# Kernel optimization log

Measured on AMD Instinct MI355X. Metric: run time of the kernel, lower is better.

Reference implementation:

```python
import jax, jax.numpy as jnp
import numpy as np

B_, L_, D_MODEL = 2, 4096, 1024
D_STATE, D_CONV, D_INNER = 64, 4, 2048
EPS = 1.1920929e-07  # torch.finfo(float32).eps, nn.RMSNorm default


def setup_inputs() -> dict:
    key = jax.random.key(0)
    ks = jax.random.split(key, 8)
    s = 0.02
    x = jax.random.normal(ks[0], (B_, L_, D_MODEL), jnp.float32)
    W_in = jax.random.normal(ks[1], (D_MODEL, 2 * D_INNER), jnp.float32) * s
    conv_w = jax.random.normal(ks[2], (D_INNER, 1, D_CONV), jnp.float32) * s  # depthwise (O,I/g,K)
    conv_b = jnp.zeros((D_INNER,), jnp.float32)
    W_x = jax.random.normal(ks[3], (D_INNER, 2 * D_STATE + D_INNER), jnp.float32) * s
    W_dt = jax.random.normal(ks[4], (D_INNER, D_INNER), jnp.float32) * s
    b_dt = jnp.zeros((D_INNER,), jnp.float32)
    A_log = jnp.log(jnp.tile(jnp.arange(1, D_STATE + 1, dtype=jnp.float32)[None, :], (D_INNER, 1)))
    D_param = jnp.ones((D_INNER,), jnp.float32)
    W_out = jax.random.normal(ks[5], (D_INNER, D_MODEL), jnp.float32) * s
    norm_w = jnp.ones((D_INNER,), jnp.float32)
    return dict(x=x, W_in=W_in, conv_w=conv_w, conv_b=conv_b, W_x=W_x, W_dt=W_dt,
                b_dt=b_dt, A_log=A_log, D_param=D_param, W_out=W_out, norm_w=norm_w)


def selective_scan(x_conv, dt, A, B_ssm, C_ssm, D_param):
    # x_conv,dt: (B,L,d_inner); A:(d_inner,d_state); B_ssm,C_ssm:(B,L,d_state)
    dt = jax.nn.softplus(dt)

    def step(h, inp):
        dt_t, B_t, C_t, x_t = inp  # (B,di),(B,ds),(B,ds),(B,di)
        dA = jnp.exp(dt_t[:, :, None] * A[None, :, :])           # (B,di,ds)
        h = dA * h + (dt_t * x_t)[:, :, None] * B_t[:, None, :]  # (B,di,ds)
        y = jnp.einsum('bds,bs->bd', h, C_t)                     # (B,di)
        return h, y

    h0 = jnp.zeros((x_conv.shape[0], A.shape[0], A.shape[1]), x_conv.dtype)
    xs = (jnp.moveaxis(dt, 1, 0), jnp.moveaxis(B_ssm, 1, 0),
          jnp.moveaxis(C_ssm, 1, 0), jnp.moveaxis(x_conv, 1, 0))
    _, ys = jax.lax.scan(step, h0, xs)
    y = jnp.moveaxis(ys, 0, 1)  # (B,L,d_inner)
    return y + x_conv * D_param[None, None, :]


def reference(x, W_in, conv_w, conv_b, W_x, W_dt, b_dt, A_log, D_param, W_out, norm_w):
    xz = x @ W_in                                    # (B,L,2*d_inner)
    x_ssm, z = jnp.split(xz, 2, axis=-1)
    # causal depthwise conv1d: left-pad d_conv-1 == torch pad-both-then-slice[:L]
    xc = jnp.swapaxes(x_ssm, 1, 2)                   # (B,d_inner,L)
    xc = jax.lax.conv_general_dilated(
        xc, conv_w, window_strides=(1,), padding=[(D_CONV - 1, 0)],
        dimension_numbers=('NCH', 'OIH', 'NCH'), feature_group_count=D_INNER)
    xc = xc + conv_b[None, :, None]
    xc = jax.nn.silu(jnp.swapaxes(xc, 1, 2))         # (B,L,d_inner)
    dbc = xc @ W_x                                   # (B,L,2*d_state+d_inner)
    B_ssm = dbc[..., :D_STATE]
    C_ssm = dbc[..., D_STATE:2 * D_STATE]
    dt = dbc[..., 2 * D_STATE:] @ W_dt + b_dt
    A = -jnp.exp(A_log)
    y = selective_scan(xc, dt, A, B_ssm, C_ssm, D_param)
    # RMSNorm then gate
    y = y * jax.lax.rsqrt(jnp.mean(y * y, axis=-1, keepdims=True) + EPS) * norm_w
    y = y * jax.nn.silu(z)
    return y @ W_out
```

## Files before the change

kernel.cpp:

```cpp
#include <hip/hip_runtime.h>
#include <hip/hip_bf16.h>

#define L_SEQ   4096
#define DMODEL  1024
#define DINNER  2048
#define DSTATE  64
#define NB      2
#define DPB     128
#define DBCS    2304
#define NROWS   (NB * L_SEQ)

typedef unsigned short u16;
typedef __attribute__((ext_vector_type(8))) short bf16x8;
typedef __attribute__((ext_vector_type(4))) float f32x4;
typedef __attribute__((ext_vector_type(2))) float f32x2;

__device__ __forceinline__ float silu_f(float x)  { return x / (1.f + __expf(-x)); }
__device__ __forceinline__ float softplus_f(float x) {
    return x > 15.f ? x : __logf(1.f + __expf(x));
}
__device__ __forceinline__ float bf2f(u16 u) { return __uint_as_float(((unsigned)u) << 16); }
__device__ __forceinline__ u16 f2bf(float f) {
    __hip_bfloat16 h = __float2bfloat16(f);
    return *reinterpret_cast<u16*>(&h);
}
__device__ __forceinline__ unsigned pack2(float a, float b) {
    return (unsigned)f2bf(a) | ((unsigned)f2bf(b) << 16);
}

__global__ __launch_bounds__(256) void f32_to_bf16_kernel(
    const float* __restrict__ in, u16* __restrict__ out)
{
    const int i = (blockIdx.x * 256 + threadIdx.x) * 4;
    float4 v = *reinterpret_cast<const float4*>(in + i);
    ushort4 o;
    o.x = f2bf(v.x); o.y = f2bf(v.y); o.z = f2bf(v.z); o.w = f2bf(v.w);
    *reinterpret_cast<ushort4*>(out + i) = o;
}

__global__ __launch_bounds__(256) void transpose_bf16_kernel(
    const float* __restrict__ W, u16* __restrict__ Wt, int K, int N)
{
    __shared__ float t[32][33];
    const int n0 = blockIdx.x * 32, k0 = blockIdx.y * 32;
    const int tx = threadIdx.x & 31, ty = threadIdx.x >> 5;
    #pragma unroll
    for (int i = 0; i < 32; i += 8)
        t[ty + i][tx] = W[(size_t)(k0 + ty + i) * N + n0 + tx];
    __syncthreads();
    #pragma unroll
    for (int i = 0; i < 32; i += 8)
        Wt[(size_t)(n0 + ty + i) * K + k0 + tx] = f2bf(t[tx][ty + i]);
}

__global__ __launch_bounds__(256) void bias_cat_kernel(
    const float* __restrict__ b_dt, float* __restrict__ bias)
{
    const int i = blockIdx.x * 256 + threadIdx.x;
    float v = 0.f;
    if (i >= 128 && i < 128 + DINNER) v = b_dt[i - 128];
    bias[i] = v;
}

template <typename TC>
__global__ __launch_bounds__(256) void mfma_gemm(
    const u16* __restrict__ A, int lda,
    const u16* __restrict__ Bt, int ldb,
    TC* __restrict__ C, int ldc,
    int K, const float* __restrict__ bias)
{
    __shared__ u16 As[128 * 32];
    __shared__ u16 Bs[128 * 32];
    const int tid  = threadIdx.x;
    const int lane = tid & 63;
    const int w    = tid >> 6;
    const int wm   = w >> 1, wn = w & 1;

    const int gx = gridDim.x;
    const int nwg = gx * gridDim.y;
    int wg = blockIdx.y * gx + blockIdx.x;
    if ((nwg & 7) == 0) wg = (wg & 7) * (nwg >> 3) + (wg >> 3);
    const int bm = (wg / gx) * 128, bn = (wg % gx) * 128;

    const int lr = lane & 15, lk = lane >> 4;
    const int srow  = lane >> 2;
    const int scolb = (lane & 3) * 16;
    const size_t ldaB = (size_t)lda * 2, ldbB = (size_t)ldb * 2;

    const char* Ab = (const char*)A + (size_t)bm * ldaB;
    const char* Bb = (const char*)Bt + (size_t)bn * ldbB;
    char* AsB = (char*)As;
    char* BsB = (char*)Bs;

    f32x4 acc[4][4] = {};

    for (int k0 = 0; k0 < K; k0 += 32) {
        const size_t kb = (size_t)k0 * 2;
        #pragma unroll
        for (int i = 0; i < 2; ++i) {
            const int row = i * 64 + w * 16 + srow;
            __builtin_amdgcn_global_load_lds(
                (const __attribute__((address_space(1))) void*)(Ab + (size_t)row * ldaB + kb + scolb),
                (__attribute__((address_space(3))) void*)(AsB + i * 4096 + w * 1024),
                16, 0, 0);
            __builtin_amdgcn_global_load_lds(
                (const __attribute__((address_space(1))) void*)(Bb + (size_t)row * ldbB + kb + scolb),
                (__attribute__((address_space(3))) void*)(BsB + i * 4096 + w * 1024),
                16, 0, 0);
        }
        __syncthreads();
        bf16x8 a[4], b[4];
        #pragma unroll
        for (int mi = 0; mi < 4; ++mi)
            a[mi] = *reinterpret_cast<const bf16x8*>(&As[(wm * 64 + mi * 16 + lr) * 32 + lk * 8]);
        #pragma unroll
        for (int ni = 0; ni < 4; ++ni)
            b[ni] = *reinterpret_cast<const bf16x8*>(&Bs[(wn * 64 + ni * 16 + lr) * 32 + lk * 8]);
        #pragma unroll
        for (int mi = 0; mi < 4; ++mi)
            #pragma unroll
            for (int ni = 0; ni < 4; ++ni)
                acc[mi][ni] = __builtin_amdgcn_mfma_f32_16x16x32_bf16(a[mi], b[ni], acc[mi][ni], 0, 0, 0);
        __syncthreads();
    }

    float bv[4];
    if (bias) {
        #pragma unroll
        for (int ni = 0; ni < 4; ++ni) bv[ni] = bias[bn + wn * 64 + ni * 16 + lr];
    }
    #pragma unroll
    for (int mi = 0; mi < 4; ++mi) {
        #pragma unroll
        for (int ni = 0; ni < 4; ++ni) {
            #pragma unroll
            for (int r = 0; r < 4; ++r) {
                const int row = bm + wm * 64 + mi * 16 + lk * 4 + r;
                const int col = bn + wn * 64 + ni * 16 + lr;
                float v = acc[mi][ni][r];
                if (bias) v += bv[ni];
                if constexpr (sizeof(TC) == 4) C[(size_t)row * ldc + col] = v;
                else                           C[(size_t)row * ldc + col] = f2bf(v);
            }
        }
    }
}

#define BAR()  asm volatile("s_barrier" ::: "memory")
#define WV(n)  asm volatile("s_waitcnt vmcnt(" #n ")" ::: "memory")
#define STG16(s, d) __builtin_amdgcn_global_load_lds( \
    (const __attribute__((address_space(1))) void*)(s), \
    (__attribute__((address_space(3))) void*)(d), 16, 0, 0)

template <typename TC, int ACT>
__global__ __launch_bounds__(512, 2) void gemm256(
    const u16* __restrict__ A, int lda,
    const u16* __restrict__ Bt, int ldb,
    TC* __restrict__ C, int ldc,
    int K, const float* __restrict__ bias)
{
    extern __shared__ char lds[];
    const int tid = threadIdx.x;
    const int l = tid & 63, w = tid >> 6;
    const int wm = w >> 2, wn = w & 3;
    const int lr = l & 15, lk = l >> 4;

    const int gx = gridDim.x;
    const int nwg = gx * gridDim.y;
    int wg = blockIdx.y * gx + blockIdx.x;
    wg = (wg & 7) * (nwg >> 3) + (wg >> 3);
    const int bm = (wg / gx) * 256, bn = (wg % gx) * 256;

    const size_t ldaB = (size_t)lda * 2, ldbB = (size_t)ldb * 2;
    const int gsw = (((l & 7) ^ (l >> 3)) << 4);
    const char* aSrc = (const char*)A + (size_t)(bm + w * 8 + (l >> 3)) * ldaB + gsw;
    const char* bSrc = (const char*)Bt + (size_t)(bn + w * 8 + (l >> 3)) * ldbB + gsw;
    const int csw0 = (lk * 16) ^ ((lr & 7) << 4);
    const int wdst = w * 1024;

    const int nk = K >> 6;
    f32x4 acc[8][4] = {};

    {
        STG16(aSrc + (size_t)(0 * 64) * ldaB, lds + 0 * 8192 + wdst);
        STG16(aSrc + (size_t)(2 * 64) * ldaB, lds + 2 * 8192 + wdst);
        STG16(bSrc + (size_t)(0 * 64) * ldbB, lds + 32768 + 0 * 8192 + wdst);
        STG16(bSrc + (size_t)(1 * 64) * ldbB, lds + 32768 + 1 * 8192 + wdst);
        STG16(bSrc + (size_t)(2 * 64) * ldbB, lds + 32768 + 2 * 8192 + wdst);
        STG16(bSrc + (size_t)(3 * 64) * ldbB, lds + 32768 + 3 * 8192 + wdst);
        STG16(aSrc + (size_t)(1 * 64) * ldaB, lds + 1 * 8192 + wdst);
        STG16(aSrc + (size_t)(3 * 64) * ldaB, lds + 3 * 8192 + wdst);
        WV(2);
        BAR();
    }

    for (int t = 0; t < nk; ++t) {
        const int p = t & 1;
        const char* Ar = lds + (p << 16);
        const char* Br = Ar + 32768;
        const int tn = (t + 1 < nk) ? t + 1 : t;
        char* dq = lds + (((t + 1) & 1) << 16);
        const size_t Tb = (size_t)tn << 7;
        const char* aS = aSrc + Tb;
        const char* bS = bSrc + Tb;

        bf16x8 a[4][2], bf[2][2];

        #pragma unroll
        for (int mi = 0; mi < 4; ++mi) {
            const int ro = (wm * 128 + mi * 16 + lr) * 128;
            a[mi][0] = *reinterpret_cast<const bf16x8*>(Ar + ro + csw0);
            a[mi][1] = *reinterpret_cast<const bf16x8*>(Ar + ro + (csw0 ^ 64));
        }
        #pragma unroll
        for (int ni = 0; ni < 2; ++ni) {
            const int ro = (wn * 64 + ni * 16 + lr) * 128;
            bf[ni][0] = *reinterpret_cast<const bf16x8*>(Br + ro + csw0);
            bf[ni][1] = *reinterpret_cast<const bf16x8*>(Br + ro + (csw0 ^ 64));
        }
        STG16(aS + (size_t)(0 * 64) * ldaB, dq + 0 * 8192 + wdst);
        STG16(aS + (size_t)(2 * 64) * ldaB, dq + 2 * 8192 + wdst);
        BAR();
        __builtin_amdgcn_s_setprio(1);
        #pragma unroll
        for (int mi = 0; mi < 4; ++mi)
            #pragma unroll
            for (int ni = 0; ni < 2; ++ni) {
                acc[mi][ni] = __builtin_amdgcn_mfma_f32_16x16x32_bf16(a[mi][0], bf[ni][0], acc[mi][ni], 0, 0, 0);
                acc[mi][ni] = __builtin_amdgcn_mfma_f32_16x16x32_bf16(a[mi][1], bf[ni][1], acc[mi][ni], 0, 0, 0);
            }
        __builtin_amdgcn_s_setprio(0);
        BAR();

        #pragma unroll
        for (int ni = 0; ni < 2; ++ni) {
            const int ro = (wn * 64 + (2 + ni) * 16 + lr) * 128;
            bf[ni][0] = *reinterpret_cast<const bf16x8*>(Br + ro + csw0);
            bf[ni][1] = *reinterpret_cast<const bf16x8*>(Br + ro + (csw0 ^ 64));
        }
        STG16(bS + (size_t)(0 * 64) * ldbB, dq + 32768 + 0 * 8192 + wdst);
        STG16(bS + (size_t)(1 * 64) * ldbB, dq + 32768 + 1 * 8192 + wdst);
        BAR();
        __builtin_amdgcn_s_setprio(1);
        #pragma unroll
        for (int mi = 0; mi < 4; ++mi)
            #pragma unroll
            for (int ni = 0; ni < 2; ++ni) {
                acc[mi][2 + ni] = __builtin_amdgcn_mfma_f32_16x16x32_bf16(a[mi][0], bf[ni][0], acc[mi][2 + ni], 0, 0, 0);
                acc[mi][2 + ni] = __builtin_amdgcn_mfma_f32_16x16x32_bf16(a[mi][1], bf[ni][1], acc[mi][2 + ni], 0, 0, 0);
            }
        __builtin_amdgcn_s_setprio(0);
        WV(4);
        BAR();

        #pragma unroll
        for (int mi = 0; mi < 4; ++mi) {
            const int ro = (wm * 128 + (4 + mi) * 16 + lr) * 128;
            a[mi][0] = *reinterpret_cast<const bf16x8*>(Ar + ro + csw0);
            a[mi][1] = *reinterpret_cast<const bf16x8*>(Ar + ro + (csw0 ^ 64));
        }
        STG16(bS + (size_t)(2 * 64) * ldbB, dq + 32768 + 2 * 8192 + wdst);
        STG16(bS + (size_t)(3 * 64) * ldbB, dq + 32768 + 3 * 8192 + wdst);
        BAR();
        __builtin_amdgcn_s_setprio(1);
        #pragma unroll
        for (int mi = 0; mi < 4; ++mi)
            #pragma unroll
            for (int ni = 0; ni < 2; ++ni) {
                acc[4 + mi][2 + ni] = __builtin_amdgcn_mfma_f32_16x16x32_bf16(a[mi][0], bf[ni][0], acc[4 + mi][2 + ni], 0, 0, 0);
                acc[4 + mi][2 + ni] = __builtin_amdgcn_mfma_f32_16x16x32_bf16(a[mi][1], bf[ni][1], acc[4 + mi][2 + ni], 0, 0, 0);
            }
        __builtin_amdgcn_s_setprio(0);
        BAR();

        #pragma unroll
        for (int ni = 0; ni < 2; ++ni) {
            const int ro = (wn * 64 + ni * 16 + lr) * 128;
            bf[ni][0] = *reinterpret_cast<const bf16x8*>(Br + ro + csw0);
            bf[ni][1] = *reinterpret_cast<const bf16x8*>(Br + ro + (csw0 ^ 64));
        }
        STG16(aS + (size_t)(1 * 64) * ldaB, dq + 1 * 8192 + wdst);
        STG16(aS + (size_t)(3 * 64) * ldaB, dq + 3 * 8192 + wdst);
        BAR();
        __builtin_amdgcn_s_setprio(1);
        #pragma unroll
        for (int mi = 0; mi < 4; ++mi)
            #pragma unroll
            for (int ni = 0; ni < 2; ++ni) {
                acc[4 + mi][ni] = __builtin_amdgcn_mfma_f32_16x16x32_bf16(a[mi][0], bf[ni][0], acc[4 + mi][ni], 0, 0, 0);
                acc[4 + mi][ni] = __builtin_amdgcn_mfma_f32_16x16x32_bf16(a[mi][1], bf[ni][1], acc[4 + mi][ni], 0, 0, 0);
            }
        __builtin_amdgcn_s_setprio(0);
        WV(2);
        BAR();
    }

    float bv[4];
    if (bias) {
        #pragma unroll
        for (int ni = 0; ni < 4; ++ni) bv[ni] = bias[bn + wn * 64 + ni * 16 + lr];
    }
    #pragma unroll
    for (int mi = 0; mi < 8; ++mi) {
        #pragma unroll
        for (int ni = 0; ni < 4; ++ni) {
            #pragma unroll
            for (int r = 0; r < 4; ++r) {
                const int row = bm + wm * 128 + mi * 16 + lk * 4 + r;
                const int col = bn + wn * 64 + ni * 16 + lr;
                float v = acc[mi][ni][r];
                if (bias) v += bv[ni];
                if constexpr (ACT == 2) { if (col >= 128) v = softplus_f(v); }
                if constexpr (sizeof(TC) == 4) C[(size_t)row * ldc + col] = v;
                else                           C[(size_t)row * ldc + col] = f2bf(v);
            }
        }
    }
}

__global__ __launch_bounds__(256) void conv_silu_kernel(
    const u16* __restrict__ xz, const float* __restrict__ cw,
    const float* __restrict__ cb, u16* __restrict__ xc)
{
    const int idx8 = blockIdx.x * 256 + threadIdx.x;
    const int db  = (idx8 & 255) << 3;
    const int row = idx8 >> 8;
    const int l   = row & (L_SEQ - 1);

    float v[4][8];
    #pragma unroll
    for (int k = 0; k < 4; ++k) {
        const int ll = l - 3 + k;
        if (ll >= 0) {
            uint4 u = *reinterpret_cast<const uint4*>(xz + (size_t)(row - 3 + k) * 4096 + db);
            v[k][0]=bf2f((u16)(u.x&0xffff)); v[k][1]=bf2f((u16)(u.x>>16));
            v[k][2]=bf2f((u16)(u.y&0xffff)); v[k][3]=bf2f((u16)(u.y>>16));
            v[k][4]=bf2f((u16)(u.z&0xffff)); v[k][5]=bf2f((u16)(u.z>>16));
            v[k][6]=bf2f((u16)(u.w&0xffff)); v[k][7]=bf2f((u16)(u.w>>16));
        } else {
            #pragma unroll
            for (int j = 0; j < 8; ++j) v[k][j] = 0.f;
        }
    }
    float acc[8];
    {
        float4 c0 = *reinterpret_cast<const float4*>(cb + db);
        float4 c1 = *reinterpret_cast<const float4*>(cb + db + 4);
        acc[0]=c0.x; acc[1]=c0.y; acc[2]=c0.z; acc[3]=c0.w;
        acc[4]=c1.x; acc[5]=c1.y; acc[6]=c1.z; acc[7]=c1.w;
    }
    #pragma unroll
    for (int j = 0; j < 8; ++j) {
        const float4 wv = reinterpret_cast<const float4*>(cw)[db + j];
        acc[j] = fmaf(v[0][j], wv.x, acc[j]);
        acc[j] = fmaf(v[1][j], wv.y, acc[j]);
        acc[j] = fmaf(v[2][j], wv.z, acc[j]);
        acc[j] = fmaf(v[3][j], wv.w, acc[j]);
    }
    uint4 o;
    o.x = pack2(silu_f(acc[0]), silu_f(acc[1]));
    o.y = pack2(silu_f(acc[2]), silu_f(acc[3]));
    o.z = pack2(silu_f(acc[4]), silu_f(acc[5]));
    o.w = pack2(silu_f(acc[6]), silu_f(acc[7]));
    *reinterpret_cast<uint4*>(xc + (size_t)row * 2048 + db) = o;
}


__device__ __forceinline__ int a_pattern_check_half(
    const float* A_log, int d, int base, float& A0)
{
    A0 = -__expf(A_log[d * DSTATE]);
    int ok = 1;
    #pragma unroll
    for (int j = 0; j < 32; ++j) {
        const int s = base + j;
        const float As = -__expf(A_log[d * DSTATE + s]);
        ok &= (fabsf(As - A0 * (float)(s + 1)) <= 1e-3f * (float)(s + 1));
    }
    return ok;
}

#define UNPACK8(dstp, u)  do {                                             \
    float4 _a, _b;                                                         \
    _a.x=bf2f((u16)((u).x&0xffff)); _a.y=bf2f((u16)((u).x>>16));           \
    _a.z=bf2f((u16)((u).y&0xffff)); _a.w=bf2f((u16)((u).y>>16));           \
    _b.x=bf2f((u16)((u).z&0xffff)); _b.y=bf2f((u16)((u).z>>16));           \
    _b.z=bf2f((u16)((u).w&0xffff)); _b.w=bf2f((u16)((u).w>>16));           \
    *reinterpret_cast<float4*>(dstp) = _a;                                 \
    *reinterpret_cast<float4*>((dstp) + 4) = _b;                           \
} while (0)

__global__ __launch_bounds__(256) void scan_phase1(
    const u16* __restrict__ xc,
    const u16* __restrict__ dbc,
    const float* __restrict__ A_log,
    float* __restrict__ hend, float* __restrict__ sumdt,
    int nchunk, int chunk)
{
    const int tid  = threadIdx.x;
    const int dl   = tid >> 1, half = tid & 1;
    const int base = half * 32;
    const int d0   = blockIdx.x * DPB;
    const int d    = d0 + dl;
    const int c = blockIdx.y, b = blockIdx.z;
    const int t0 = c * chunk;
    const size_t bL = (size_t)b * L_SEQ;

    __shared__ float dts_s[16][132];
    __shared__ float xcs_s[16][132];
    __shared__ float Bs_s[16][68];

    float A0;
    int fast = a_pattern_check_half(A_log, d, base, A0);
    fast = __syncthreads_and(fast);

    f32x2 h2[16];
    #pragma unroll
    for (int j = 0; j < 16; ++j) h2[j] = (f32x2){0.f, 0.f};
    float sd = 0.f;

    for (int ts = 0; ts < chunk; ts += 16) {
        __syncthreads();
        {
            const int rr = tid >> 4, cc = (tid & 15) * 8;
            const size_t row = bL + t0 + ts + rr;
            uint4 v = *reinterpret_cast<const uint4*>(dbc + row * DBCS + 128 + d0 + cc);
            UNPACK8(&dts_s[rr][cc], v);
            uint4 u = *reinterpret_cast<const uint4*>(xc + row * 2048 + d0 + cc);
            UNPACK8(&xcs_s[rr][cc], u);
        }
        if (tid < 128) {
            const int rr = tid >> 3, cc = (tid & 7) * 8;
            const size_t row = bL + t0 + ts + rr;
            uint4 v = *reinterpret_cast<const uint4*>(dbc + row * DBCS + cc);
            UNPACK8(&Bs_s[rr][cc], v);
        }
        __syncthreads();
        if (fast) {
            for (int r = 0; r < 16; ++r) {
                const float dts = dts_s[r][dl];
                const float xv  = xcs_s[r][dl];
                const float dtx = dts * xv;
                sd += dts;
                const float q  = __expf(A0 * dts);
                const float q2 = q * q, q3 = q2 * q, q4 = q2 * q2;
                const float q8 = q4 * q4, q16 = q8 * q8, q32 = q16 * q16;
                const float qb = half ? q32 : 1.f;
                f32x2 pA = {qb * q, qb * q2};
                f32x2 pB = {qb * q3, qb * q4};
                const f32x2 q44 = {q4, q4};
                const f32x2 dtx2 = {dtx, dtx};
                #pragma unroll
                for (int g = 0; g < 8; ++g) {
                    const f32x2 B01 = *reinterpret_cast<const f32x2*>(&Bs_s[r][base + g * 4]);
                    const f32x2 B23 = *reinterpret_cast<const f32x2*>(&Bs_s[r][base + g * 4 + 2]);
                    h2[2*g]   = pA * h2[2*g]   + B01 * dtx2;
                    h2[2*g+1] = pB * h2[2*g+1] + B23 * dtx2;
                    pA = pA * q44; pB = pB * q44;
                }
            }
        } else {
            float* hs = (float*)h2;
            for (int r = 0; r < 16; ++r) {
                const float dts = dts_s[r][dl];
                const float xv  = xcs_s[r][dl];
                const float dtx = dts * xv;
                sd += dts;
                #pragma unroll
                for (int j = 0; j < 32; ++j) {
                    const float a = __expf(-__expf(A_log[d * DSTATE + base + j]) * dts);
                    hs[j] = fmaf(a, hs[j], dtx * Bs_s[r][base + j]);
                }
            }
        }
    }
    const size_t cb64 = ((size_t)b * nchunk + c) * DSTATE;
    const float* hs = (const float*)h2;
    #pragma unroll
    for (int j = 0; j < 32; ++j) hend[(cb64 + base + j) * DINNER + d] = hs[j];
    if (half == 0) sumdt[((size_t)b * nchunk + c) * DINNER + d] = sd;
}

__global__ __launch_bounds__(256) void scan_phase2(
    float* __restrict__ hbuf, const float* __restrict__ sumdt,
    const float* __restrict__ A_log, int nchunk)
{
    const int idx = blockIdx.x * 256 + threadIdx.x;
    const int d = idx & (DINNER - 1);
    const int s = (idx >> 11) & (DSTATE - 1);
    const int b = idx >> 17;

    const float A = -__expf(A_log[d * DSTATE + s]);
    float h = 0.f;
    for (int c = 0; c < nchunk; ++c) {
        const size_t off = (((size_t)b * nchunk + c) * DSTATE + s) * DINNER + d;
        const float he = hbuf[off];
        const float ap = __expf(A * sumdt[((size_t)b * nchunk + c) * DINNER + d]);
        hbuf[off] = h;
        h = fmaf(ap, h, he);
    }
}

__global__ __launch_bounds__(256) void scan_phase3(
    u16* __restrict__ xc,
    const u16* __restrict__ dbc,
    const float* __restrict__ A_log,
    const float* __restrict__ hinit,
    const float* __restrict__ D_param,
    int nchunk, int chunk)
{
    const int tid  = threadIdx.x;
    const int dl   = tid >> 1, half = tid & 1;
    const int base = half * 32;
    const int d0   = blockIdx.x * DPB;
    const int d    = d0 + dl;
    const int c = blockIdx.y, b = blockIdx.z;
    const int t0 = c * chunk;
    const size_t bL = (size_t)b * L_SEQ;

    __shared__ float dts_s[16][132];
    __shared__ float xcs_s[16][132];
    __shared__ float BCs[16][132];

    float A0;
    int fast = a_pattern_check_half(A_log, d, base, A0);
    fast = __syncthreads_and(fast);

    f32x2 h2[16];
    {
        const size_t cb64 = ((size_t)b * nchunk + c) * DSTATE;
        float* hs = (float*)h2;
        #pragma unroll
        for (int j = 0; j < 32; ++j) hs[j] = hinit[(cb64 + base + j) * DINNER + d];
    }
    const float Dp = D_param[d];

    for (int ts = 0; ts < chunk; ts += 16) {
        __syncthreads();
        {
            const int rr = tid >> 4, cc = (tid & 15) * 8;
            const size_t row = bL + t0 + ts + rr;
            uint4 v = *reinterpret_cast<const uint4*>(dbc + row * DBCS + 128 + d0 + cc);
            UNPACK8(&dts_s[rr][cc], v);
            uint4 u = *reinterpret_cast<const uint4*>(xc + row * 2048 + d0 + cc);
            UNPACK8(&xcs_s[rr][cc], u);
            uint4 w = *reinterpret_cast<const uint4*>(dbc + row * DBCS + cc);
            UNPACK8(&BCs[rr][cc], w);
        }
        __syncthreads();
        if (fast) {
            for (int r = 0; r < 16; ++r) {
                const float dts = dts_s[r][dl];
                const float xv  = xcs_s[r][dl];
                const float dtx = dts * xv;
                const float q  = __expf(A0 * dts);
                const float q2 = q * q, q3 = q2 * q, q4 = q2 * q2;
                const float q8 = q4 * q4, q16 = q8 * q8, q32 = q16 * q16;
                const float qb = half ? q32 : 1.f;
                f32x2 pA = {qb * q, qb * q2};
                f32x2 pB = {qb * q3, qb * q4};
                const f32x2 q44 = {q4, q4};
                const f32x2 dtx2 = {dtx, dtx};
                f32x2 y2 = {0.f, 0.f};
                #pragma unroll
                for (int g = 0; g < 8; ++g) {
                    const f32x2 B01 = *reinterpret_cast<const f32x2*>(&BCs[r][base + g * 4]);
                    const f32x2 B23 = *reinterpret_cast<const f32x2*>(&BCs[r][base + g * 4 + 2]);
                    const f32x2 C01 = *reinterpret_cast<const f32x2*>(&BCs[r][64 + base + g * 4]);
                    const f32x2 C23 = *reinterpret_cast<const f32x2*>(&BCs[r][64 + base + g * 4 + 2]);
                    h2[2*g]   = pA * h2[2*g]   + B01 * dtx2;
                    h2[2*g+1] = pB * h2[2*g+1] + B23 * dtx2;
                    y2 = h2[2*g] * C01 + y2;
                    y2 = h2[2*g+1] * C23 + y2;
                    pA = pA * q44; pB = pB * q44;
                }
                float y = y2.x + y2.y;
                const float yt = y + __shfl_xor(y, 1, 64);
                if (half == 0) {
                    const size_t row = bL + t0 + ts + r;
                    xc[row * 2048 + d] = f2bf(fmaf(xv, Dp, yt));
                }
            }
        } else {
            float* hs = (float*)h2;
            for (int r = 0; r < 16; ++r) {
                const float dts = dts_s[r][dl];
                const float xv  = xcs_s[r][dl];
                const float dtx = dts * xv;
                float y = 0.f;
                #pragma unroll
                for (int j = 0; j < 32; ++j) {
                    const float a = __expf(-__expf(A_log[d * DSTATE + base + j]) * dts);
                    hs[j] = fmaf(a, hs[j], dtx * BCs[r][base + j]);
                    y = fmaf(hs[j], BCs[r][64 + base + j], y);
                }
                const float yt = y + __shfl_xor(y, 1, 64);
                if (half == 0) {
                    const size_t row = bL + t0 + ts + r;
                    xc[row * 2048 + d] = f2bf(fmaf(xv, Dp, yt));
                }
            }
        }
    }
}

__global__ __launch_bounds__(256) void rms_gate_kernel(
    u16* __restrict__ y, const u16* __restrict__ xz,
    const float* __restrict__ norm_w)
{
    const int row = blockIdx.x;
    const int tid = threadIdx.x;
    const size_t ybase = (size_t)row * DINNER;
    const size_t zbase = (size_t)row * 4096 + DINNER;
    const int i8 = tid * 8;

    float yv[8];
    {
        uint4 u = *reinterpret_cast<const uint4*>(y + ybase + i8);
        yv[0]=bf2f((u16)(u.x&0xffff)); yv[1]=bf2f((u16)(u.x>>16));
        yv[2]=bf2f((u16)(u.y&0xffff)); yv[3]=bf2f((u16)(u.y>>16));
        yv[4]=bf2f((u16)(u.z&0xffff)); yv[5]=bf2f((u16)(u.z>>16));
        yv[6]=bf2f((u16)(u.w&0xffff)); yv[7]=bf2f((u16)(u.w>>16));
    }
    float ss = 0.f;
    #pragma unroll
    for (int j = 0; j < 8; ++j) ss = fmaf(yv[j], yv[j], ss);
    #pragma unroll
    for (int off = 32; off > 0; off >>= 1) ss += __shfl_down(ss, off, 64);
    __shared__ float sred[4];
    const int lane = tid & 63, wid = tid >> 6;
    if (lane == 0) sred[wid] = ss;
    __syncthreads();
    const float tot = sred[0] + sred[1] + sred[2] + sred[3];
    const float scale = rsqrtf(tot * (1.f / (float)DINNER) + 1.1920929e-07f);

    float zv[8];
    {
        uint4 u = *reinterpret_cast<const uint4*>(xz + zbase + i8);
        zv[0]=bf2f((u16)(u.x&0xffff)); zv[1]=bf2f((u16)(u.x>>16));
        zv[2]=bf2f((u16)(u.y&0xffff)); zv[3]=bf2f((u16)(u.y>>16));
        zv[4]=bf2f((u16)(u.z&0xffff)); zv[5]=bf2f((u16)(u.z>>16));
        zv[6]=bf2f((u16)(u.w&0xffff)); zv[7]=bf2f((u16)(u.w>>16));
    }
    float4 n0 = *reinterpret_cast<const float4*>(norm_w + i8);
    float4 n1 = *reinterpret_cast<const float4*>(norm_w + i8 + 4);
    const float nw[8] = {n0.x,n0.y,n0.z,n0.w,n1.x,n1.y,n1.z,n1.w};
    float o[8];
    #pragma unroll
    for (int j = 0; j < 8; ++j) o[j] = yv[j] * scale * nw[j] * silu_f(zv[j]);
    uint4 ov;
    ov.x = pack2(o[0], o[1]); ov.y = pack2(o[2], o[3]);
    ov.z = pack2(o[4], o[5]); ov.w = pack2(o[6], o[7]);
    *reinterpret_cast<uint4*>(y + ybase + i8) = ov;
}

extern "C" void kernel_launch(void* const* d_in, const int* in_sizes, int n_in,
                              void* d_out, int out_size, void* d_ws, size_t ws_size,
                              hipStream_t stream)
{
    const float* x       = (const float*)d_in[0];
    const float* W_in    = (const float*)d_in[1];
    const float* conv_w  = (const float*)d_in[2];
    const float* conv_b  = (const float*)d_in[3];
    const float* W_x     = (const float*)d_in[4];
    const float* W_dt    = (const float*)d_in[5];
    const float* b_dt    = (const float*)d_in[6];
    const float* A_log   = (const float*)d_in[7];
    const float* D_param = (const float*)d_in[8];
    const float* W_out   = (const float*)d_in[9];
    const float* norm_w  = (const float*)d_in[10];
    float* out = (float*)d_out;

    hipFuncSetAttribute(reinterpret_cast<const void*>(&gemm256<u16, 0>),
                        hipFuncAttributeMaxDynamicSharedMemorySize, 131072);
    hipFuncSetAttribute(reinterpret_cast<const void*>(&gemm256<u16, 2>),
                        hipFuncAttributeMaxDynamicSharedMemorySize, 131072);

    char* ws = (char*)d_ws;
    u16* xz  = (u16*)(ws);
    u16* xc  = (u16*)(ws + 67108864ull);
    u16* dbc = (u16*)(ws + 100663296ull);
    u16* xbf  = dbc;
    u16* Wxbf = xz;
    u16* Wt_out = (u16*)(ws + 138412032ull);
    float* bias2304 = (float*)(ws + 142606336ull);
    const size_t fixed_bytes = 142615552ull;
    const size_t per_chunk = 2ull * DSTATE * DINNER * 4 + 2ull * DINNER * 4;
    int nchunk = 64;
    while (nchunk > 1 && fixed_bytes + (size_t)nchunk * per_chunk > ws_size) nchunk >>= 1;
    const int chunk = L_SEQ / nchunk;
    float* hbuf = (float*)(ws + fixed_bytes);
    float* sdt  = (float*)(ws + fixed_bytes + (size_t)nchunk * 2ull * DSTATE * DINNER * 4);

    u16* Wt_in = (u16*)d_out;
    u16* Wt_x  = Wt_in + 4194304ull;
    u16* Wt_dt = Wt_x + 4718592ull;

    const int M = NROWS;

    f32_to_bf16_kernel<<<(M * DMODEL) / 1024, 256, 0, stream>>>(x, xbf);
    f32_to_bf16_kernel<<<(DINNER * 2176) / 1024, 256, 0, stream>>>(W_x, Wxbf);
    transpose_bf16_kernel<<<dim3(4096 / 32, 1024 / 32), 256, 0, stream>>>(W_in, Wt_in, 1024, 4096);
    transpose_bf16_kernel<<<dim3(4, 2048 / 32), 256, 0, stream>>>(W_x, Wt_x, 2048, 2176);
    transpose_bf16_kernel<<<dim3(2048 / 32, 2048 / 32), 256, 0, stream>>>(W_dt, Wt_dt, 2048, 2048);
    transpose_bf16_kernel<<<dim3(1024 / 32, 2048 / 32), 256, 0, stream>>>(W_out, Wt_out, 2048, 1024);
    bias_cat_kernel<<<9, 256, 0, stream>>>(b_dt, bias2304);
    hipMemsetAsync(Wt_x + 2176ull * 2048, 0, 128ull * 2048 * 2, stream);
    mfma_gemm<u16><<<dim3(2048 / 128, 2048 / 128), 256, 0, stream>>>(
        Wt_dt, 2048, Wxbf + 128, 2176, Wt_x + 128ull * 2048, 2048, 2048, nullptr);

    gemm256<u16, 0><<<dim3(4096 / 256, M / 256), 512, 131072, stream>>>(
        xbf, DMODEL, Wt_in, DMODEL, xz, 4096, DMODEL, nullptr);
    conv_silu_kernel<<<(M * DINNER) / (256 * 8), 256, 0, stream>>>(xz, conv_w, conv_b, xc);
    gemm256<u16, 2><<<dim3(DBCS / 256, M / 256), 512, 131072, stream>>>(
        xc, DINNER, Wt_x, DINNER, dbc, DBCS, DINNER, bias2304);
    scan_phase1<<<dim3(DINNER / DPB, nchunk, NB), 256, 0, stream>>>(
        xc, dbc, A_log, hbuf, sdt, nchunk, chunk);
    scan_phase2<<<(NB * DINNER * DSTATE) / 256, 256, 0, stream>>>(hbuf, sdt, A_log, nchunk);
    scan_phase3<<<dim3(DINNER / DPB, nchunk, NB), 256, 0, stream>>>(
        xc, dbc, A_log, hbuf, D_param, nchunk, chunk);
    rms_gate_kernel<<<M, 256, 0, stream>>>(xc, xz, norm_w);
    mfma_gemm<float><<<dim3(1024 / 128, M / 128), 256, 0, stream>>>(
        xc, DINNER, Wt_out, DINNER, out, DMODEL, DINNER, nullptr);
}
```

Measured before the change: 654.0 us.

## Double-buffer scan tiles with register prefetch in scan phases 1 and 3

Both chunked-scan kernels now keep two shared-memory tile buffers. The next 16-row tile of dt, xc and B/C is loaded into registers before computing on the current tile, then written to the alternate buffer afterwards, so each step needs one barrier instead of two. This is meant to hide global-load latency behind the sequential recurrence. It also switches the B/C LDS reads to 128-bit vector loads. The cost is twice the shared memory and more live registers, which may lower occupancy. Phase 3 writes its y output into the xc buffer at rows the prefetch does not read, so the prefetch stays safe.

```diff
diff --git a/kernel.cpp b/kernel.cpp
--- a/kernel.cpp
+++ b/kernel.cpp
@@ -406,9 +406,9 @@
     const int t0 = c * chunk;
     const size_t bL = (size_t)b * L_SEQ;
 
-    __shared__ float dts_s[16][132];
-    __shared__ float xcs_s[16][132];
-    __shared__ float Bs_s[16][68];
+    __shared__ float dts_s[2][16][132];
+    __shared__ float xcs_s[2][16][132];
+    __shared__ float Bs_s[2][16][68];
 
     float A0;
     int fast = a_pattern_check_half(A_log, d, base, A0);
@@ -419,27 +419,36 @@
     for (int j = 0; j < 16; ++j) h2[j] = (f32x2){0.f, 0.f};
     float sd = 0.f;
 
+    const int rr = tid >> 4, cc = (tid & 15) * 8;
+    const int rb = tid >> 3, cb = (tid & 7) * 8;
+
+    uint4 vd, vx, vb;
+    {
+        const size_t row = bL + t0 + rr;
+        vd = *reinterpret_cast<const uint4*>(dbc + row * DBCS + 128 + d0 + cc);
+        vx = *reinterpret_cast<const uint4*>(xc + row * 2048 + d0 + cc);
+        if (tid < 128)
+            vb = *reinterpret_cast<const uint4*>(dbc + (bL + t0 + rb) * DBCS + cb);
+    }
+    UNPACK8(&dts_s[0][rr][cc], vd);
+    UNPACK8(&xcs_s[0][rr][cc], vx);
+    if (tid < 128) UNPACK8(&Bs_s[0][rb][cb], vb);
+    __syncthreads();
+
+    int cur = 0;
     for (int ts = 0; ts < chunk; ts += 16) {
-        __syncthreads();
-        {
-            const int rr = tid >> 4, cc = (tid & 15) * 8;
-            const size_t row = bL + t0 + ts + rr;
-            uint4 v = *reinterpret_cast<const uint4*>(dbc + row * DBCS + 128 + d0 + cc);
-            UNPACK8(&dts_s[rr][cc], v);
-            uint4 u = *reinterpret_cast<const uint4*>(xc + row * 2048 + d0 + cc);
-            UNPACK8(&xcs_s[rr][cc], u);
-        }
-        if (tid < 128) {
-            const int rr = tid >> 3, cc = (tid & 7) * 8;
-            const size_t row = bL + t0 + ts + rr;
-            uint4 v = *reinterpret_cast<const uint4*>(dbc + row * DBCS + cc);
-            UNPACK8(&Bs_s[rr][cc], v);
-        }
-        __syncthreads();
+        const int more = (ts + 16 < chunk);
+        if (more) {
+            const size_t row = bL + t0 + ts + 16 + rr;
+            vd = *reinterpret_cast<const uint4*>(dbc + row * DBCS + 128 + d0 + cc);
+            vx = *reinterpret_cast<const uint4*>(xc + row * 2048 + d0 + cc);
+            if (tid < 128)
+                vb = *reinterpret_cast<const uint4*>(dbc + (bL + t0 + ts + 16 + rb) * DBCS + cb);
+        }
         if (fast) {
             for (int r = 0; r < 16; ++r) {
-                const float dts = dts_s[r][dl];
-                const float xv  = xcs_s[r][dl];
+                const float dts = dts_s[cur][r][dl];
+                const float xv  = xcs_s[cur][r][dl];
                 const float dtx = dts * xv;
                 sd += dts;
                 const float q  = __expf(A0 * dts);
@@ -452,8 +461,9 @@
                 const f32x2 dtx2 = {dtx, dtx};
                 #pragma unroll
                 for (int g = 0; g < 8; ++g) {
-                    const f32x2 B01 = *reinterpret_cast<const f32x2*>(&Bs_s[r][base + g * 4]);
-                    const f32x2 B23 = *reinterpret_cast<const f32x2*>(&Bs_s[r][base + g * 4 + 2]);
+                    const f32x4 Bq = *reinterpret_cast<const f32x4*>(&Bs_s[cur][r][base + g * 4]);
+                    const f32x2 B01 = {Bq[0], Bq[1]};
+                    const f32x2 B23 = {Bq[2], Bq[3]};
                     h2[2*g]   = pA * h2[2*g]   + B01 * dtx2;
                     h2[2*g+1] = pB * h2[2*g+1] + B23 * dtx2;
                     pA = pA * q44; pB = pB * q44;
@@ -462,17 +472,24 @@
         } else {
             float* hs = (float*)h2;
             for (int r = 0; r < 16; ++r) {
-                const float dts = dts_s[r][dl];
-                const float xv  = xcs_s[r][dl];
+                const float dts = dts_s[cur][r][dl];
+                const float xv  = xcs_s[cur][r][dl];
                 const float dtx = dts * xv;
                 sd += dts;
                 #pragma unroll
                 for (int j = 0; j < 32; ++j) {
                     const float a = __expf(-__expf(A_log[d * DSTATE + base + j]) * dts);
-                    hs[j] = fmaf(a, hs[j], dtx * Bs_s[r][base + j]);
+                    hs[j] = fmaf(a, hs[j], dtx * Bs_s[cur][r][base + j]);
                 }
             }
         }
+        if (more) {
+            UNPACK8(&dts_s[cur ^ 1][rr][cc], vd);
+            UNPACK8(&xcs_s[cur ^ 1][rr][cc], vx);
+            if (tid < 128) UNPACK8(&Bs_s[cur ^ 1][rb][cb], vb);
+        }
+        __syncthreads();
+        cur ^= 1;
     }
     const size_t cb64 = ((size_t)b * nchunk + c) * DSTATE;
     const float* hs = (const float*)h2;
@@ -518,9 +535,9 @@
     const int t0 = c * chunk;
     const size_t bL = (size_t)b * L_SEQ;
 
-    __shared__ float dts_s[16][132];
-    __shared__ float xcs_s[16][132];
-    __shared__ float BCs[16][132];
+    __shared__ float dts_s[2][16][132];
+    __shared__ float xcs_s[2][16][132];
+    __shared__ float BCs[2][16][132];
 
     float A0;
     int fast = a_pattern_check_half(A_log, d, base, A0);
@@ -535,23 +552,33 @@
     }
     const float Dp = D_param[d];
 
+    const int rr = tid >> 4, cc = (tid & 15) * 8;
+
+    uint4 vd, vx, vw;
+    {
+        const size_t row = bL + t0 + rr;
+        vd = *reinterpret_cast<const uint4*>(dbc + row * DBCS + 128 + d0 + cc);
+        vx = *reinterpret_cast<const uint4*>(xc + row * 2048 + d0 + cc);
+        vw = *reinterpret_cast<const uint4*>(dbc + row * DBCS + cc);
+    }
+    UNPACK8(&dts_s[0][rr][cc], vd);
+    UNPACK8(&xcs_s[0][rr][cc], vx);
+    UNPACK8(&BCs[0][rr][cc], vw);
+    __syncthreads();
+
+    int cur = 0;
     for (int ts = 0; ts < chunk; ts += 16) {
-        __syncthreads();
-        {
-            const int rr = tid >> 4, cc = (tid & 15) * 8;
-            const size_t row = bL + t0 + ts + rr;
-            uint4 v = *reinterpret_cast<const uint4*>(dbc + row * DBCS + 128 + d0 + cc);
-            UNPACK8(&dts_s[rr][cc], v);
-            uint4 u = *reinterpret_cast<const uint4*>(xc + row * 2048 + d0 + cc);
-            UNPACK8(&xcs_s[rr][cc], u);
-            uint4 w = *reinterpret_cast<const uint4*>(dbc + row * DBCS + cc);
-            UNPACK8(&BCs[rr][cc], w);
-        }
-        __syncthreads();
+        const int more = (ts + 16 < chunk);
+        if (more) {
+            const size_t row = bL + t0 + ts + 16 + rr;
+            vd = *reinterpret_cast<const uint4*>(dbc + row * DBCS + 128 + d0 + cc);
+            vx = *reinterpret_cast<const uint4*>(xc + row * 2048 + d0 + cc);
+            vw = *reinterpret_cast<const uint4*>(dbc + row * DBCS + cc);
+        }
         if (fast) {
             for (int r = 0; r < 16; ++r) {
-                const float dts = dts_s[r][dl];
-                const float xv  = xcs_s[r][dl];
+                const float dts = dts_s[cur][r][dl];
+                const float xv  = xcs_s[cur][r][dl];
                 const float dtx = dts * xv;
                 const float q  = __expf(A0 * dts);
                 const float q2 = q * q, q3 = q2 * q, q4 = q2 * q2;
@@ -564,10 +591,12 @@
                 f32x2 y2 = {0.f, 0.f};
                 #pragma unroll
                 for (int g = 0; g < 8; ++g) {
-                    const f32x2 B01 = *reinterpret_cast<const f32x2*>(&BCs[r][base + g * 4]);
-                    const f32x2 B23 = *reinterpret_cast<const f32x2*>(&BCs[r][base + g * 4 + 2]);
-                    const f32x2 C01 = *reinterpret_cast<const f32x2*>(&BCs[r][64 + base + g * 4]);
-                    const f32x2 C23 = *reinterpret_cast<const f32x2*>(&BCs[r][64 + base + g * 4 + 2]);
+                    const f32x4 Bq = *reinterpret_cast<const f32x4*>(&BCs[cur][r][base + g * 4]);
+                    const f32x4 Cq = *reinterpret_cast<const f32x4*>(&BCs[cur][r][64 + base + g * 4]);
+                    const f32x2 B01 = {Bq[0], Bq[1]};
+                    const f32x2 B23 = {Bq[2], Bq[3]};
+                    const f32x2 C01 = {Cq[0], Cq[1]};
+                    const f32x2 C23 = {Cq[2], Cq[3]};
                     h2[2*g]   = pA * h2[2*g]   + B01 * dtx2;
                     h2[2*g+1] = pB * h2[2*g+1] + B23 * dtx2;
                     y2 = h2[2*g] * C01 + y2;
@@ -584,15 +613,15 @@
         } else {
             float* hs = (float*)h2;
             for (int r = 0; r < 16; ++r) {
-                const float dts = dts_s[r][dl];
-                const float xv  = xcs_s[r][dl];
+                const float dts = dts_s[cur][r][dl];
+                const float xv  = xcs_s[cur][r][dl];
                 const float dtx = dts * xv;
                 float y = 0.f;
                 #pragma unroll
                 for (int j = 0; j < 32; ++j) {
                     const float a = __expf(-__expf(A_log[d * DSTATE + base + j]) * dts);
-                    hs[j] = fmaf(a, hs[j], dtx * BCs[r][base + j]);
-                    y = fmaf(hs[j], BCs[r][64 + base + j], y);
+                    hs[j] = fmaf(a, hs[j], dtx * BCs[cur][r][base + j]);
+                    y = fmaf(hs[j], BCs[cur][r][64 + base + j], y);
                 }
                 const float yt = y + __shfl_xor(y, 1, 64);
                 if (half == 0) {
@@ -601,6 +630,13 @@
                 }
             }
         }
+        if (more) {
+            UNPACK8(&dts_s[cur ^ 1][rr][cc], vd);
+            UNPACK8(&xcs_s[cur ^ 1][rr][cc], vx);
+            UNPACK8(&BCs[cur ^ 1][rr][cc], vw);
+        }
+        __syncthreads();
+        cur ^= 1;
     }
 }
 
```

After: 673.0 us. 2.9% more time.
